# Optimization experiments

Hardware: AMD Instinct MI355X
Metric: run time of the kernel (lower is better)

Reference implementation:

```python
import jax, jax.numpy as jnp
import numpy as np

IN_DIM, INTER_DIM, OUT_DIM = 512, 256, 512


def setup_inputs() -> dict:
    key = jax.random.key(0)
    k1, k2, k3, k4 = jax.random.split(key, 4)
    feat_map = jax.random.normal(k1, (8, IN_DIM, 64, 64), dtype=jnp.float32)
    # xavier-uniform-style init scales
    lim_p = float(np.sqrt(6.0 / (IN_DIM + INTER_DIM)))
    lim_w = float(np.sqrt(6.0 / (IN_DIM + OUT_DIM)))
    phi_w = jax.random.uniform(k2, (INTER_DIM, IN_DIM), jnp.float32, -lim_p, lim_p)
    theta_w = jax.random.uniform(k3, (INTER_DIM, IN_DIM), jnp.float32, -lim_p, lim_p)
    weight = jax.random.uniform(k4, (IN_DIM, OUT_DIM), jnp.float32, -lim_w, lim_w)
    return {"feat_map": feat_map, "phi_w": phi_w, "theta_w": theta_w, "weight": weight}


def reference(feat_map, phi_w, theta_w, weight):
    B, D, H, W = feat_map.shape
    # b c h w -> b (h w) c
    feat_vec = jnp.transpose(feat_map.reshape(B, D, H * W), (0, 2, 1))  # [B, HW, D]
    phi = jnp.einsum('bnc,ic->bni', feat_vec, phi_w)      # [B, HW, inter]
    theta = jnp.einsum('bnc,ic->bni', feat_vec, theta_w)  # [B, HW, inter]
    product = jnp.einsum('bni,bmi->bnm', phi, theta)      # [B, HW, HW]
    phi_norm = jnp.linalg.norm(phi, axis=-1, keepdims=True)      # [B, HW, 1]
    theta_norm = jnp.linalg.norm(theta, axis=-1, keepdims=True)  # [B, HW, 1]
    norms = phi_norm * jnp.transpose(theta_norm, (0, 2, 1))      # [B, HW, HW]
    sim = jax.nn.softmax(product / norms, axis=-1)
    out = jnp.einsum('bnm,bmc->bnc', sim, feat_vec)  # [B, HW, D]
    out = jnp.einsum('bnc,cd->bnd', out, weight)     # [B, HW, out_dim]
    # b (h w) d -> b d h w
    updated = jnp.transpose(out, (0, 2, 1)).reshape(B, -1, H, W)
    return jax.nn.relu(updated)
```

## Files before the change

kernel.cpp:

```cpp
#include <hip/hip_runtime.h>


typedef short s8v __attribute__((ext_vector_type(8)));
typedef float f4v __attribute__((ext_vector_type(4)));

__device__ inline ushort f2bf(float x) {
  union { float f; unsigned u; } v; v.f = x;
  unsigned u = v.u + 0x7fff + ((v.u >> 16) & 1);
  return (ushort)(u >> 16);
}

__global__ __launch_bounds__(256) void k0(const float* __restrict__ feat,
                                          const float* __restrict__ pw,
                                          const float* __restrict__ tw,
                                          const float* __restrict__ w,
                                          ushort* __restrict__ featT,
                                          ushort* __restrict__ featV,
                                          ushort* __restrict__ wbp,
                                          ushort* __restrict__ wbt,
                                          ushort* __restrict__ wT) {
  int bid = blockIdx.x;
  int t = threadIdx.x;
  __shared__ ushort tile[64][72];

  if (bid < 4096) {
    int b = bid >> 9, cb = (bid >> 6) & 7, mt = bid & 63;
#pragma unroll
    for (int p = 0; p < 4; p++) {
      int ci = p * 16 + (t >> 4);
      int mi = (t & 15) * 4;
      float4 v = *(const float4*)&feat[((size_t)(b * 512 + cb * 64 + ci)) * 4096 + mt * 64 + mi];
      ushort4 u; u.x = f2bf(v.x); u.y = f2bf(v.y); u.z = f2bf(v.z); u.w = f2bf(v.w);
      *(ushort4*)&featV[((size_t)(b * 64 + mt) * 512 + cb * 64 + ci) * 64 + mi] = u;
      tile[ci][mi] = u.x; tile[ci][mi + 1] = u.y; tile[ci][mi + 2] = u.z; tile[ci][mi + 3] = u.w;
    }
    __syncthreads();
    int m = t >> 2, cs = (t & 3) * 16;
    ushort tmp[16];
#pragma unroll
    for (int j = 0; j < 16; j++) tmp[j] = tile[cs + j][m];
    ushort* dst = &featT[((size_t)(b * 4096 + mt * 64 + m)) * 512 + cb * 64 + cs];
    *(s8v*)dst = *(s8v*)&tmp[0];
    *(s8v*)(dst + 8) = *(s8v*)&tmp[8];
  } else if (bid < 4352) {
    int bb = bid - 4096;
    const float* src = (bb < 128) ? pw : tw;
    ushort* dst = (bb < 128) ? wbp : wbt;
    int idx = ((bb & 127) * 256 + t) * 4;
    float4 v = *(const float4*)&src[idx];
    ushort4 u; u.x = f2bf(v.x); u.y = f2bf(v.y); u.z = f2bf(v.z); u.w = f2bf(v.w);
    *(ushort4*)&dst[idx] = u;
  } else {
    int bb = bid - 4352;
    int cb = bb >> 3, db = bb & 7;
#pragma unroll
    for (int p = 0; p < 4; p++) {
      int ci = p * 16 + (t >> 4);
      int di = (t & 15) * 4;
      float4 v = *(const float4*)&w[(size_t)(cb * 64 + ci) * 512 + db * 64 + di];
      tile[ci][di] = f2bf(v.x); tile[ci][di + 1] = f2bf(v.y);
      tile[ci][di + 2] = f2bf(v.z); tile[ci][di + 3] = f2bf(v.w);
    }
    __syncthreads();
    int d = t >> 2, cs = (t & 3) * 16;
    ushort tmp[16];
#pragma unroll
    for (int j = 0; j < 16; j++) tmp[j] = tile[cs + j][d];
    ushort* dst = &wT[(size_t)(db * 64 + d) * 512 + cb * 64 + cs];
    *(s8v*)dst = *(s8v*)&tmp[0];
    *(s8v*)(dst + 8) = *(s8v*)&tmp[8];
  }
}

__global__ __launch_bounds__(512) void k1_gemm(
    const ushort* __restrict__ featT, const ushort* __restrict__ wbp,
    const ushort* __restrict__ wbt, ushort* __restrict__ phi_n,
    ushort* __restrict__ theta_n) {
  int bid = blockIdx.x;
  int b = bid & 7;
  int rest = bid >> 3;
  int half = rest & 1;
  int nt = rest >> 1;
  const ushort* wb = half ? wbt : wbp;
  ushort* dst = half ? theta_n : phi_n;
  int t = threadIdx.x;
  int lane = t & 63, w = t >> 6;
  int col = lane & 15, quad = lane >> 4;
  int wn = w >> 2, wi = w & 3;
  int nb = nt * 128 + wn * 64;

  __shared__ float part[128][4];

  const ushort* ab = featT + ((size_t)(b * 4096 + nb + col)) * 512 + quad * 8;
  const ushort* bb = wb + ((size_t)(wi * 64 + col)) * 512 + quad * 8;

  f4v acc[16];
#pragma unroll
  for (int i = 0; i < 16; i++) acc[i] = (f4v){0.f, 0.f, 0.f, 0.f};

  s8v afA[4], bfA[4], afB[4], bfB[4];
#pragma unroll
  for (int rs = 0; rs < 4; rs++) afA[rs] = *(const s8v*)(ab + (size_t)(rs * 16) * 512);
#pragma unroll
  for (int ct = 0; ct < 4; ct++) bfA[ct] = *(const s8v*)(bb + (size_t)(ct * 16) * 512);

#pragma unroll 1
  for (int kc = 0; kc < 16; kc += 2) {
#pragma unroll
    for (int rs = 0; rs < 4; rs++)
      afB[rs] = *(const s8v*)(ab + (size_t)(rs * 16) * 512 + (kc + 1) * 32);
#pragma unroll
    for (int ct = 0; ct < 4; ct++)
      bfB[ct] = *(const s8v*)(bb + (size_t)(ct * 16) * 512 + (kc + 1) * 32);
#pragma unroll
    for (int rs = 0; rs < 4; rs++)
#pragma unroll
      for (int ct = 0; ct < 4; ct++)
        acc[rs * 4 + ct] =
            __builtin_amdgcn_mfma_f32_16x16x32_bf16(afA[rs], bfA[ct], acc[rs * 4 + ct], 0, 0, 0);
    if (kc + 2 < 16) {
#pragma unroll
      for (int rs = 0; rs < 4; rs++)
        afA[rs] = *(const s8v*)(ab + (size_t)(rs * 16) * 512 + (kc + 2) * 32);
#pragma unroll
      for (int ct = 0; ct < 4; ct++)
        bfA[ct] = *(const s8v*)(bb + (size_t)(ct * 16) * 512 + (kc + 2) * 32);
    }
#pragma unroll
    for (int rs = 0; rs < 4; rs++)
#pragma unroll
      for (int ct = 0; ct < 4; ct++)
        acc[rs * 4 + ct] =
            __builtin_amdgcn_mfma_f32_16x16x32_bf16(afB[rs], bfB[ct], acc[rs * 4 + ct], 0, 0, 0);
  }

#pragma unroll
  for (int rs = 0; rs < 4; rs++) {
#pragma unroll
    for (int reg = 0; reg < 4; reg++) {
      float ss = 0.f;
#pragma unroll
      for (int ct = 0; ct < 4; ct++) {
        float v = acc[rs * 4 + ct][reg];
        ss += v * v;
      }
      ss += __shfl_xor(ss, 1); ss += __shfl_xor(ss, 2);
      ss += __shfl_xor(ss, 4); ss += __shfl_xor(ss, 8);
      if (col == 0) part[wn * 64 + rs * 16 + quad * 4 + reg][wi] = ss;
    }
  }
  __syncthreads();

  float rinv[4][4];
#pragma unroll
  for (int rs = 0; rs < 4; rs++) {
#pragma unroll
    for (int reg = 0; reg < 4; reg++) {
      float4 p = *(const float4*)&part[wn * 64 + rs * 16 + quad * 4 + reg][0];
      rinv[rs][reg] = rsqrtf(p.x + p.y + p.z + p.w);
    }
  }

#pragma unroll
  for (int rs = 0; rs < 4; rs++) {
#pragma unroll
    for (int ct = 0; ct < 4; ct++) {
#pragma unroll
      for (int reg = 0; reg < 4; reg++) {
        dst[((size_t)(b * 4096 + nb + rs * 16 + quad * 4 + reg)) * 256 +
            wi * 64 + ct * 16 + col] = f2bf(acc[rs * 4 + ct][reg] * rinv[rs][reg]);
      }
    }
  }
}

__global__ __launch_bounds__(512, 2) void k3_attn(
    const ushort* __restrict__ phi_n, const ushort* __restrict__ theta_n,
    const ushort* __restrict__ featV, ushort* __restrict__ out1) {
  int bid = blockIdx.x;
  int b = bid & 7;
  int n0 = (bid >> 3) << 6;
  int t = threadIdx.x;
  int lane = t & 63, w = t >> 6;
  int col = lane & 15, quad = lane >> 4;
  int mh4 = w & 3, rh = w >> 2;
  int l32 = lane & 31, h32 = lane >> 5;
  int cs = col & 7;

  __shared__ __align__(16) ushort ks[2 * 16384];
  __shared__ __align__(16) ushort ps[2 * 4096];
  __shared__ float dred[4 * 64];

  s8v qfA[8], qfB[8];
  {
    const ushort* qa = phi_n + ((size_t)(b * 4096 + n0 + rh * 32 + col)) * 256 + quad * 8;
#pragma unroll
    for (int f = 0; f < 8; f++) qfA[f] = *(const s8v*)(qa + f * 32);
    const ushort* qb = qa + 16 * 256;
#pragma unroll
    for (int f = 0; f < 8; f++) qfB[f] = *(const s8v*)(qb + f * 32);
  }

  const ushort* thb = theta_n + (size_t)b * 4096 * 256;
  const ushort* vbb = featV + (size_t)b * 64 * 512 * 64 + (size_t)(w * 64) * 64;

  f4v acc[16];
#pragma unroll
  for (int i = 0; i < 16; i++) acc[i] = (f4v){0.f, 0.f, 0.f, 0.f};
  float denp[8] = {0.f, 0.f, 0.f, 0.f, 0.f, 0.f, 0.f, 0.f};

#pragma unroll
  for (int u = 0; u < 4; u++) {
    int row = w * 8 + u * 2 + h32;
    s8v val = *(const s8v*)(thb + (size_t)row * 256 + l32 * 8);
    *(s8v*)(ks + row * 256 + ((l32 ^ (row & 7)) * 8)) = val;
  }
  __syncthreads();

#pragma unroll 1
  for (int mt = 0; mt < 64; mt++) {
    const ushort* kc_ = ks + (mt & 1) * 16384;
    ushort* kn_ = ks + ((mt & 1) ^ 1) * 16384;
    ushort* pw_ = ps + (mt & 1) * 4096;

    s8v kreg[4];
    if (mt < 63) {
      int m1 = (mt + 1) << 6;
#pragma unroll
      for (int u = 0; u < 4; u++) {
        int row = w * 8 + u * 2 + h32;
        kreg[u] = *(const s8v*)(thb + (size_t)(m1 + row) * 256 + l32 * 8);
      }
    }
    s8v v0[4], v1[4];
    {
      const ushort* vb = vbb + (size_t)mt * 32768;
#pragma unroll
      for (int ct = 0; ct < 4; ct++) {
        const ushort* p = vb + (ct * 16 + col) * 64 + quad * 8;
        v0[ct] = *(const s8v*)p;
        v1[ct] = *(const s8v*)(p + 32);
      }
    }

    f4v svA0 = (f4v){0.f, 0.f, 0.f, 0.f}, svA1 = (f4v){0.f, 0.f, 0.f, 0.f};
    f4v svB0 = (f4v){0.f, 0.f, 0.f, 0.f}, svB1 = (f4v){0.f, 0.f, 0.f, 0.f};
    {
      const ushort* kb = kc_ + (mh4 * 16 + col) * 256;
      __builtin_amdgcn_s_setprio(1);
#pragma unroll
      for (int kk = 0; kk < 8; kk += 2) {
        int pos0 = ((kk * 4 + quad) ^ cs) * 8;
        int pos1 = (((kk + 1) * 4 + quad) ^ cs) * 8;
        s8v bf0 = *(const s8v*)(kb + pos0);
        s8v bf1 = *(const s8v*)(kb + pos1);
        svA0 = __builtin_amdgcn_mfma_f32_16x16x32_bf16(qfA[kk], bf0, svA0, 0, 0, 0);
        svB0 = __builtin_amdgcn_mfma_f32_16x16x32_bf16(qfB[kk], bf0, svB0, 0, 0, 0);
        svA1 = __builtin_amdgcn_mfma_f32_16x16x32_bf16(qfA[kk + 1], bf1, svA1, 0, 0, 0);
        svB1 = __builtin_amdgcn_mfma_f32_16x16x32_bf16(qfB[kk + 1], bf1, svB1, 0, 0, 0);
      }
      __builtin_amdgcn_s_setprio(0);
    }

    float pA[4], pB[4];
#pragma unroll
    for (int r = 0; r < 4; r++) {
      pA[r] = __expf(svA0[r] + svA1[r]);
      pB[r] = __expf(svB0[r] + svB1[r]);
      denp[r] += pA[r];
      denp[4 + r] += pB[r];
    }

    {
      int j0 = mh4 * 2 + (col >> 3);
#pragma unroll
      for (int r = 0; r < 4; r++) {
        int nA = rh * 32 + quad * 4 + r;
        pw_[nA * 64 + ((j0 ^ (nA & 7)) * 8) + cs] = f2bf(pA[r]);
        int nB = nA + 16;
        pw_[nB * 64 + ((j0 ^ (nB & 7)) * 8) + cs] = f2bf(pB[r]);
      }
    }
    if (mt < 63) {
#pragma unroll
      for (int u = 0; u < 4; u++) {
        int row = w * 8 + u * 2 + h32;
        *(s8v*)(kn_ + row * 256 + ((l32 ^ (row & 7)) * 8)) = kreg[u];
      }
    }
    asm volatile("s_waitcnt lgkmcnt(0)" ::: "memory");
    __builtin_amdgcn_s_barrier();

    __builtin_amdgcn_s_setprio(1);
#pragma unroll
    for (int rs = 0; rs < 4; rs++) {
      const ushort* pb = pw_ + (rs * 16 + col) * 64;
      s8v pf0 = *(const s8v*)(pb + ((quad ^ cs) * 8));
      s8v pf1 = *(const s8v*)(pb + (((quad + 4) ^ cs) * 8));
#pragma unroll
      for (int ct = 0; ct < 4; ct++) {
        acc[rs * 4 + ct] =
            __builtin_amdgcn_mfma_f32_16x16x32_bf16(pf0, v0[ct], acc[rs * 4 + ct], 0, 0, 0);
        acc[rs * 4 + ct] =
            __builtin_amdgcn_mfma_f32_16x16x32_bf16(pf1, v1[ct], acc[rs * 4 + ct], 0, 0, 0);
      }
    }
    __builtin_amdgcn_s_setprio(0);
  }

#pragma unroll
  for (int i = 0; i < 8; i++) {
    float d = denp[i];
    d += __shfl_xor(d, 1); d += __shfl_xor(d, 2);
    d += __shfl_xor(d, 4); d += __shfl_xor(d, 8);
    denp[i] = d;
  }
  if (col == 0) {
#pragma unroll
    for (int i = 0; i < 8; i++) {
      int n = rh * 32 + (i >> 2) * 16 + quad * 4 + (i & 3);
      dred[mh4 * 64 + n] = denp[i];
    }
  }
  __syncthreads();
  if (t < 64) dred[t] = 1.0f / (dred[t] + dred[64 + t] + dred[128 + t] + dred[192 + t]);
  __syncthreads();

#pragma unroll
  for (int rs = 0; rs < 4; rs++) {
#pragma unroll
    for (int ct = 0; ct < 4; ct++) {
#pragma unroll
      for (int reg = 0; reg < 4; reg++) {
        int n = rs * 16 + quad * 4 + reg;
        out1[((size_t)(b * 4096 + n0 + n)) * 512 + w * 64 + ct * 16 + col] =
            f2bf(acc[rs * 4 + ct][reg] * dred[n]);
      }
    }
  }
}

__global__ __launch_bounds__(512) void k4_out(
    const ushort* __restrict__ out1, const ushort* __restrict__ wT,
    float* __restrict__ out) {
  int bid = blockIdx.x;
  int b = bid & 7;
  int rest = bid >> 3;
  int dt = rest & 3;
  int nt = rest >> 2;
  int t = threadIdx.x;
  int lane = t & 63, w = t >> 6;
  int col = lane & 15, quad = lane >> 4;
  int dw = w & 1, nw = w >> 1;
  int d0 = dt * 128 + dw * 64;
  int n0 = nt * 256 + nw * 64;

  const ushort* ab = wT + (size_t)(d0 + col) * 512 + quad * 8;
  const ushort* bb = out1 + ((size_t)(b * 4096 + n0 + col)) * 512 + quad * 8;

  f4v acc[16];
#pragma unroll
  for (int i = 0; i < 16; i++) acc[i] = (f4v){0.f, 0.f, 0.f, 0.f};

  s8v afA[4], bfA[4], afB[4], bfB[4];
#pragma unroll
  for (int rs = 0; rs < 4; rs++) afA[rs] = *(const s8v*)(ab + (size_t)(rs * 16) * 512);
#pragma unroll
  for (int ct = 0; ct < 4; ct++) bfA[ct] = *(const s8v*)(bb + (size_t)(ct * 16) * 512);

#pragma unroll 1
  for (int kc = 0; kc < 16; kc += 2) {
#pragma unroll
    for (int rs = 0; rs < 4; rs++)
      afB[rs] = *(const s8v*)(ab + (size_t)(rs * 16) * 512 + (kc + 1) * 32);
#pragma unroll
    for (int ct = 0; ct < 4; ct++)
      bfB[ct] = *(const s8v*)(bb + (size_t)(ct * 16) * 512 + (kc + 1) * 32);
#pragma unroll
    for (int rs = 0; rs < 4; rs++)
#pragma unroll
      for (int ct = 0; ct < 4; ct++)
        acc[rs * 4 + ct] =
            __builtin_amdgcn_mfma_f32_16x16x32_bf16(afA[rs], bfA[ct], acc[rs * 4 + ct], 0, 0, 0);
    if (kc + 2 < 16) {
#pragma unroll
      for (int rs = 0; rs < 4; rs++)
        afA[rs] = *(const s8v*)(ab + (size_t)(rs * 16) * 512 + (kc + 2) * 32);
#pragma unroll
      for (int ct = 0; ct < 4; ct++)
        bfA[ct] = *(const s8v*)(bb + (size_t)(ct * 16) * 512 + (kc + 2) * 32);
    }
#pragma unroll
    for (int rs = 0; rs < 4; rs++)
#pragma unroll
      for (int ct = 0; ct < 4; ct++)
        acc[rs * 4 + ct] =
            __builtin_amdgcn_mfma_f32_16x16x32_bf16(afB[rs], bfB[ct], acc[rs * 4 + ct], 0, 0, 0);
  }

#pragma unroll
  for (int rs = 0; rs < 4; rs++) {
#pragma unroll
    for (int ct = 0; ct < 4; ct++) {
#pragma unroll
      for (int reg = 0; reg < 4; reg++) {
        int d = d0 + rs * 16 + quad * 4 + reg;
        int n = n0 + ct * 16 + col;
        out[((size_t)(b * 512 + d)) * 4096 + n] = fmaxf(acc[rs * 4 + ct][reg], 0.f);
      }
    }
  }
}

extern "C" void kernel_launch(void* const* d_in, const int* in_sizes, int n_in,
                              void* d_out, int out_size, void* d_ws, size_t ws_size,
                              hipStream_t stream) {
  const float* feat    = (const float*)d_in[0];
  const float* phi_w   = (const float*)d_in[1];
  const float* theta_w = (const float*)d_in[2];
  const float* weight  = (const float*)d_in[3];
  float* out = (float*)d_out;

  ushort* wsu = (ushort*)d_ws;
  ushort* featT   = wsu;
  ushort* featV   = wsu + 16777216;
  ushort* phi_n   = wsu + 33554432;
  ushort* theta_n = wsu + 41943040;
  ushort* wbp     = wsu + 50331648;
  ushort* wbt     = wsu + 50462720;
  ushort* weightT = wsu + 50593792;
  ushort* out1    = wsu;

  k0<<<dim3(4416), dim3(256), 0, stream>>>(feat, phi_w, theta_w, weight,
                                           featT, featV, wbp, wbt, weightT);
  k1_gemm<<<dim3(512), dim3(512), 0, stream>>>(featT, wbp, wbt, phi_n, theta_n);
  k3_attn<<<dim3(512), dim3(512), 0, stream>>>(phi_n, theta_n, featV, out1);
  k4_out<<<dim3(512), dim3(512), 0, stream>>>(out1, weightT, out);
}
```

Baseline: 530.4 us.

## Fuse output projection GEMM into attention kernel via swizzled LDS tile

The attention kernel now writes its normalized 64x512 bf16 output tile into shared memory using an XOR-swizzled layout, instead of writing it to global memory. It then multiplies that tile by the transposed weight directly, applies ReLU, and stores the final fp32 result. This removes the separate output kernel and the global round trip of the intermediate activations. In exchange, each block loads the full 512x512 weight from global/L2 with no LDS reuse, and the attention kernel grows longer, with more register pressure under the 2-waves-per-SIMD launch bound.

```diff
diff --git a/kernel.cpp b/kernel.cpp
--- a/kernel.cpp
+++ b/kernel.cpp
@@ -176,7 +176,8 @@
 
 __global__ __launch_bounds__(512, 2) void k3_attn(
     const ushort* __restrict__ phi_n, const ushort* __restrict__ theta_n,
-    const ushort* __restrict__ featV, ushort* __restrict__ out1) {
+    const ushort* __restrict__ featV, const ushort* __restrict__ wT,
+    float* __restrict__ out) {
   int bid = blockIdx.x;
   int b = bid & 7;
   int n0 = (bid >> 3) << 6;
@@ -330,83 +331,51 @@
   for (int rs = 0; rs < 4; rs++) {
 #pragma unroll
     for (int ct = 0; ct < 4; ct++) {
+      int c = w * 64 + ct * 16 + col;
+      int chunk = c >> 3;
 #pragma unroll
       for (int reg = 0; reg < 4; reg++) {
         int n = rs * 16 + quad * 4 + reg;
-        out1[((size_t)(b * 4096 + n0 + n)) * 512 + w * 64 + ct * 16 + col] =
+        ks[n * 512 + ((chunk ^ (n & 7)) * 8) + (c & 7)] =
             f2bf(acc[rs * 4 + ct][reg] * dred[n]);
       }
     }
   }
-}
-
-__global__ __launch_bounds__(512) void k4_out(
-    const ushort* __restrict__ out1, const ushort* __restrict__ wT,
-    float* __restrict__ out) {
-  int bid = blockIdx.x;
-  int b = bid & 7;
-  int rest = bid >> 3;
-  int dt = rest & 3;
-  int nt = rest >> 2;
-  int t = threadIdx.x;
-  int lane = t & 63, w = t >> 6;
-  int col = lane & 15, quad = lane >> 4;
-  int dw = w & 1, nw = w >> 1;
-  int d0 = dt * 128 + dw * 64;
-  int n0 = nt * 256 + nw * 64;
-
-  const ushort* ab = wT + (size_t)(d0 + col) * 512 + quad * 8;
-  const ushort* bb = out1 + ((size_t)(b * 4096 + n0 + col)) * 512 + quad * 8;
-
-  f4v acc[16];
-#pragma unroll
-  for (int i = 0; i < 16; i++) acc[i] = (f4v){0.f, 0.f, 0.f, 0.f};
-
-  s8v afA[4], bfA[4], afB[4], bfB[4];
-#pragma unroll
-  for (int rs = 0; rs < 4; rs++) afA[rs] = *(const s8v*)(ab + (size_t)(rs * 16) * 512);
-#pragma unroll
-  for (int ct = 0; ct < 4; ct++) bfA[ct] = *(const s8v*)(bb + (size_t)(ct * 16) * 512);
-
-#pragma unroll 1
-  for (int kc = 0; kc < 16; kc += 2) {
-#pragma unroll
-    for (int rs = 0; rs < 4; rs++)
-      afB[rs] = *(const s8v*)(ab + (size_t)(rs * 16) * 512 + (kc + 1) * 32);
-#pragma unroll
-    for (int ct = 0; ct < 4; ct++)
-      bfB[ct] = *(const s8v*)(bb + (size_t)(ct * 16) * 512 + (kc + 1) * 32);
-#pragma unroll
-    for (int rs = 0; rs < 4; rs++)
-#pragma unroll
-      for (int ct = 0; ct < 4; ct++)
-        acc[rs * 4 + ct] =
-            __builtin_amdgcn_mfma_f32_16x16x32_bf16(afA[rs], bfA[ct], acc[rs * 4 + ct], 0, 0, 0);
-    if (kc + 2 < 16) {
+  __syncthreads();
+
+  {
+    const ushort* ab = wT + (size_t)(w * 64 + col) * 512 + quad * 8;
+    f4v acc2[16];
+#pragma unroll
+    for (int i = 0; i < 16; i++) acc2[i] = (f4v){0.f, 0.f, 0.f, 0.f};
+#pragma unroll 2
+    for (int kc = 0; kc < 16; kc++) {
+      s8v af[4], bf[4];
 #pragma unroll
       for (int rs = 0; rs < 4; rs++)
-        afA[rs] = *(const s8v*)(ab + (size_t)(rs * 16) * 512 + (kc + 2) * 32);
-#pragma unroll
-      for (int ct = 0; ct < 4; ct++)
-        bfA[ct] = *(const s8v*)(bb + (size_t)(ct * 16) * 512 + (kc + 2) * 32);
-    }
-#pragma unroll
-    for (int rs = 0; rs < 4; rs++)
-#pragma unroll
-      for (int ct = 0; ct < 4; ct++)
-        acc[rs * 4 + ct] =
-            __builtin_amdgcn_mfma_f32_16x16x32_bf16(afB[rs], bfB[ct], acc[rs * 4 + ct], 0, 0, 0);
-  }
-
-#pragma unroll
-  for (int rs = 0; rs < 4; rs++) {
-#pragma unroll
-    for (int ct = 0; ct < 4; ct++) {
-#pragma unroll
-      for (int reg = 0; reg < 4; reg++) {
-        int d = d0 + rs * 16 + quad * 4 + reg;
-        int n = n0 + ct * 16 + col;
-        out[((size_t)(b * 512 + d)) * 4096 + n] = fmaxf(acc[rs * 4 + ct][reg], 0.f);
+        af[rs] = *(const s8v*)(ab + (size_t)(rs * 16) * 512 + kc * 32);
+#pragma unroll
+      for (int ct = 0; ct < 4; ct++) {
+        int n = ct * 16 + col;
+        bf[ct] = *(const s8v*)(ks + n * 512 + (((kc * 4 + quad) ^ cs) * 8));
+      }
+#pragma unroll
+      for (int rs = 0; rs < 4; rs++)
+#pragma unroll
+        for (int ct = 0; ct < 4; ct++)
+          acc2[rs * 4 + ct] =
+              __builtin_amdgcn_mfma_f32_16x16x32_bf16(af[rs], bf[ct], acc2[rs * 4 + ct], 0, 0, 0);
+    }
+#pragma unroll
+    for (int rs = 0; rs < 4; rs++) {
+#pragma unroll
+      for (int ct = 0; ct < 4; ct++) {
+#pragma unroll
+        for (int reg = 0; reg < 4; reg++) {
+          int d = w * 64 + rs * 16 + quad * 4 + reg;
+          int n = n0 + ct * 16 + col;
+          out[((size_t)(b * 512 + d)) * 4096 + n] = fmaxf(acc2[rs * 4 + ct][reg], 0.f);
+        }
       }
     }
   }
@@ -429,11 +398,9 @@
   ushort* wbp     = wsu + 50331648;
   ushort* wbt     = wsu + 50462720;
   ushort* weightT = wsu + 50593792;
-  ushort* out1    = wsu;
 
   k0<<<dim3(4416), dim3(256), 0, stream>>>(feat, phi_w, theta_w, weight,
                                            featT, featV, wbp, wbt, weightT);
   k1_gemm<<<dim3(512), dim3(512), 0, stream>>>(featT, wbp, wbt, phi_n, theta_n);
-  k3_attn<<<dim3(512), dim3(512), 0, stream>>>(phi_n, theta_n, featV, out1);
-  k4_out<<<dim3(512), dim3(512), 0, stream>>>(out1, weightT, out);
+  k3_attn<<<dim3(512), dim3(512), 0, stream>>>(phi_n, theta_n, featV, weightT, out);
 }
```

Measured after the change: 503.5 us. -5.1%, faster.
